# Kernel tuning notes

Hardware: AMD Instinct MI355X
Metric: run time of the kernel (lower is better)

The kernel has to match this reference:

```python
import jax, jax.numpy as jnp
import numpy as np

NUM_RAYS = 65536
N_COARSE = 64
INTERS_FINE = 128


def setup_inputs() -> dict:
    key = jax.random.key(0)
    k1, k2, k3 = jax.random.split(key, 3)
    weights = jax.random.uniform(k1, (NUM_RAYS, N_COARSE), dtype=jnp.float32)
    # sorted bin edges in [2, 6), turned into contiguous intervals [start, end]
    t_edges = jnp.sort(2.0 + 4.0 * jax.random.uniform(k2, (NUM_RAYS, N_COARSE + 1), dtype=jnp.float32), axis=-1)
    t_inters = jnp.stack([t_edges[:, :-1], t_edges[:, 1:]], axis=-1)  # [R, N, 2]
    # stratified jittered u, exactly as the original np.random construction
    eps32 = np.finfo(np.float32).eps
    s = 1.0 / (INTERS_FINE + 1)
    base = jnp.arange(INTERS_FINE + 1, dtype=jnp.float32) * s  # [F+1]
    jitter = jax.random.uniform(k3, (NUM_RAYS, INTERS_FINE + 1), dtype=jnp.float32,
                                minval=0.0, maxval=s - eps32)
    u = jnp.minimum(base[None, :] + jitter, 1.0 - eps32)
    return {"weights": weights, "t_inters": t_inters, "u": u}


def reference(weights, t_inters, u):
    eps = 1e-05
    num_rays = weights.shape[0]
    # maxblur of weights (mip-NeRF style) + floor
    wp = jnp.concatenate([weights[:, :1], weights, weights[:, -1:]], axis=-1)
    wmax = jnp.maximum(wp[:, :-1], wp[:, 1:])
    w = (wmax[:, :-1] + wmax[:, 1:]) * 0.5 + 0.01  # [R, N]
    # bin edges
    t_vals = jnp.concatenate([t_inters[..., 0], t_inters[:, -1:, 1]], axis=-1)  # [R, N+1]
    # normalize to pdf with eps padding
    wsum = jnp.sum(w, axis=-1, keepdims=True)
    padding = jnp.maximum(0.0, eps - wsum)
    w = w + padding / w.shape[-1]
    wsum = wsum + padding
    pdf = w / wsum
    cdf = jnp.minimum(1.0, jnp.cumsum(pdf[..., :-1], axis=-1))
    cdf = jnp.concatenate([jnp.zeros((num_rays, 1), jnp.float32), cdf,
                           jnp.ones((num_rays, 1), jnp.float32)], axis=-1)  # [R, N+1]
    # inverse CDF: the original's broadcast mask + max/min reductions are exactly
    # searchsorted(cdf, u, side='right'); idx-1 = last bin with cdf <= u (since
    # cdf[:,0]=0 <= u and u < 1 = cdf[:,-1], indices are always interior).
    idx = jax.vmap(lambda c, uu: jnp.searchsorted(c, uu, side='right'))(cdf, u)  # [R, F+1]
    last = cdf.shape[-1] - 1
    i0 = jnp.clip(idx - 1, 0, last)
    i1 = jnp.clip(idx, 0, last)
    cdf_g0 = jnp.take_along_axis(cdf, i0, axis=-1)
    cdf_g1 = jnp.take_along_axis(cdf, i1, axis=-1)
    bins_g0 = jnp.take_along_axis(t_vals, i0, axis=-1)
    bins_g1 = jnp.take_along_axis(t_vals, i1, axis=-1)
    t = (u - cdf_g0) / (cdf_g1 - cdf_g0)
    t = jnp.where(jnp.isnan(t), 0.0, t)  # matches t[t != t] = 0
    t = jnp.clip(t, 0.0, 1.0)
    samples = bins_g0 + t * (bins_g1 - bins_g0)  # [R, F+1]
    samples = jax.lax.stop_gradient(samples)     # matches .detach()
    samples = jnp.sort(samples, axis=-1)
    return jnp.stack([samples[:, :-1], samples[:, 1:]], axis=-1)  # [R, F, 2]
```

## Files before the change

### kernel.cpp

```cpp
#include <hip/hip_runtime.h>


#define RAYS_PER_BLOCK 4

template <int CTRL, int ROW_MASK>
__device__ __forceinline__ float dpp_add(float x) {
    int sh = __builtin_amdgcn_update_dpp(0, __float_as_int(x), CTRL, ROW_MASK, 0xf, false);
    return x + __int_as_float(sh);
}

__device__ __forceinline__ float readlane_f(float v, int lane) {
    return __int_as_float(__builtin_amdgcn_readlane(__float_as_int(v), lane));
}

__device__ __forceinline__ float bperm(int byteaddr, float v) {
    return __int_as_float(__builtin_amdgcn_ds_bpermute(byteaddr, __float_as_int(v)));
}

__device__ __forceinline__ float invert_fast(float uu, float cdfv, float tix, float dtv,
                                             float c8, float c16, float c24, float c32,
                                             float c40, float c48, float c56) {
    int lo = 0;
    float clo = 0.0f, chi = 1.0f;
    bool g1 = (c32 <= uu);
    if (g1) { lo = 32; clo = c32; } else { chi = c32; }
    float cA = g1 ? c48 : c16;
    bool g2 = (cA <= uu);
    if (g2) { lo += 16; clo = cA; } else { chi = cA; }
    float pL = g1 ? c40 : c8;
    float pH = g1 ? c56 : c24;
    float cB = g2 ? pH : pL;
    bool g3 = (cB <= uu);
    if (g3) { lo += 8; clo = cB; } else { chi = cB; }
    int loB = lo << 2;
    {
        float c = bperm(loB + 12, cdfv);
        if (c <= uu) { loB += 16; clo = c; } else { chi = c; }
    }
    {
        float c = bperm(loB + 4, cdfv);
        if (c <= uu) { loB += 8; clo = c; } else { chi = c; }
    }
    {
        float c = bperm(loB, cdfv);
        if (c <= uu) { loB += 4; clo = c; } else { chi = c; }
    }
    float b0 = bperm(loB, tix);
    float dt = bperm(loB, dtv);
    float t = (uu - clo) * __builtin_amdgcn_rcpf(chi - clo);
    t = (t != t) ? 0.0f : t;
    return b0 + t * dt;
}

__global__ __launch_bounds__(64 * RAYS_PER_BLOCK)
void sample_pdf_kernel(const float* __restrict__ weights,
                       const float* __restrict__ t_inters,
                       const float* __restrict__ u,
                       float* __restrict__ out,
                       int R) {
    const int lane = threadIdx.x & 63;
    const int wave = threadIdx.x >> 6;
    const int ray  = blockIdx.x * RAYS_PER_BLOCK + wave;
    if (ray >= R) return;

    float  w  = weights[(long)ray * 64 + lane];
    float2 ti = ((const float2*)t_inters)[(long)ray * 64 + lane];
    const float* ub = u + (long)ray * 129;
    float u0 = ub[lane];
    float u1 = ub[lane + 64];
    float u2 = ub[128];

    float wm1 = __shfl_up(w, 1, 64);
    float wp1 = __shfl_down(w, 1, 64);
    if (lane == 0)  wm1 = w;
    if (lane == 63) wp1 = w;
    float w2 = (fmaxf(wm1, w) + fmaxf(w, wp1)) * 0.5f + 0.01f;

    float scan = w2;
    scan = dpp_add<0x111, 0xf>(scan);
    scan = dpp_add<0x112, 0xf>(scan);
    scan = dpp_add<0x114, 0xf>(scan);
    scan = dpp_add<0x118, 0xf>(scan);
    scan = dpp_add<0x142, 0xa>(scan);
    scan = dpp_add<0x143, 0xc>(scan);

    float wsum    = readlane_f(scan, 63);
    float padding = fmaxf(0.0f, 1e-5f - wsum);
    float invden  = __builtin_amdgcn_rcpf(wsum + padding);
    float cdfv    = fminf(1.0f, (scan + (float)(lane + 1) * (padding * (1.0f / 64.0f))) * invden);
    if (lane == 63) cdfv = 1.0f;

    float nx  = __shfl_down(ti.x, 1, 64);
    float dtv = ((lane == 63) ? ti.y : nx) - ti.x;

    float c8  = readlane_f(cdfv, 7),  c16 = readlane_f(cdfv, 15);
    float c24 = readlane_f(cdfv, 23), c32 = readlane_f(cdfv, 31);
    float c40 = readlane_f(cdfv, 39), c48 = readlane_f(cdfv, 47);
    float c56 = readlane_f(cdfv, 55);

    float s0 = invert_fast(u0, cdfv, ti.x, dtv, c8, c16, c24, c32, c40, c48, c56);
    float s1 = invert_fast(u1, cdfv, ti.x, dtv, c8, c16, c24, c32, c40, c48, c56);

    unsigned long long mask = __ballot(cdfv <= u2);
    int l2 = __builtin_amdgcn_readfirstlane(__popcll(mask));
    float clo2 = (l2 == 0) ? 0.0f : readlane_f(cdfv, (l2 - 1) & 63);
    float chi2 = readlane_f(cdfv, l2);
    float b02  = readlane_f(ti.x, l2);
    float dt2  = readlane_f(dtv,  l2);
    float t2 = (u2 - clo2) * __builtin_amdgcn_rcpf(chi2 - clo2);
    t2 = (t2 != t2) ? 0.0f : t2;
    float s2 = b02 + t2 * dt2;

    float n0 = __shfl_down(s0, 1, 64);
    if (lane == 63) n0 = readlane_f(s1, 0);
    float n1 = __shfl_down(s1, 1, 64);
    if (lane == 63) n1 = s2;

    float2* o = ((float2*)out) + (long)ray * 128;
    o[lane]      = make_float2(s0, n0);
    o[lane + 64] = make_float2(s1, n1);
}

extern "C" void kernel_launch(void* const* d_in, const int* in_sizes, int n_in,
                              void* d_out, int out_size, void* d_ws, size_t ws_size,
                              hipStream_t stream) {
    const float* weights  = (const float*)d_in[0];
    const float* t_inters = (const float*)d_in[1];
    const float* u        = (const float*)d_in[2];
    float* out            = (float*)d_out;

    const int R = in_sizes[0] / 64;
    const int grid = (R + RAYS_PER_BLOCK - 1) / RAYS_PER_BLOCK;
    sample_pdf_kernel<<<grid, 64 * RAYS_PER_BLOCK, 0, stream>>>(weights, t_inters, u, out, R);
}
```

Baseline: 30.82 us.

## Precompute per-bin affine coefficients, interleave sample ownership, use wave DPP shifts

```diff
diff --git a/kernel.cpp b/kernel.cpp
--- a/kernel.cpp
+++ b/kernel.cpp
@@ -2,11 +2,19 @@
 
 
 #define RAYS_PER_BLOCK 4
+#define DPP_WAVE_SHL1 0x130
+#define DPP_WAVE_SHR1 0x138
 
 template <int CTRL, int ROW_MASK>
 __device__ __forceinline__ float dpp_add(float x) {
     int sh = __builtin_amdgcn_update_dpp(0, __float_as_int(x), CTRL, ROW_MASK, 0xf, false);
     return x + __int_as_float(sh);
+}
+
+template <int CTRL>
+__device__ __forceinline__ float dpp_old_f(float old, float src) {
+    return __int_as_float(__builtin_amdgcn_update_dpp(
+        __float_as_int(old), __float_as_int(src), CTRL, 0xf, 0xf, false));
 }
 
 __device__ __forceinline__ float readlane_f(float v, int lane) {
@@ -17,39 +25,25 @@
     return __int_as_float(__builtin_amdgcn_ds_bpermute(byteaddr, __float_as_int(v)));
 }
 
-__device__ __forceinline__ float invert_fast(float uu, float cdfv, float tix, float dtv,
-                                             float c8, float c16, float c24, float c32,
-                                             float c40, float c48, float c56) {
-    int lo = 0;
-    float clo = 0.0f, chi = 1.0f;
+__device__ __forceinline__ int search6(float uu, float cdfv,
+                                       float c8, float c16, float c24, float c32,
+                                       float c40, float c48, float c56) {
     bool g1 = (c32 <= uu);
-    if (g1) { lo = 32; clo = c32; } else { chi = c32; }
+    int loB = g1 ? 128 : 0;
     float cA = g1 ? c48 : c16;
     bool g2 = (cA <= uu);
-    if (g2) { lo += 16; clo = cA; } else { chi = cA; }
+    loB += g2 ? 64 : 0;
     float pL = g1 ? c40 : c8;
     float pH = g1 ? c56 : c24;
     float cB = g2 ? pH : pL;
-    bool g3 = (cB <= uu);
-    if (g3) { lo += 8; clo = cB; } else { chi = cB; }
-    int loB = lo << 2;
-    {
-        float c = bperm(loB + 12, cdfv);
-        if (c <= uu) { loB += 16; clo = c; } else { chi = c; }
-    }
-    {
-        float c = bperm(loB + 4, cdfv);
-        if (c <= uu) { loB += 8; clo = c; } else { chi = c; }
-    }
-    {
-        float c = bperm(loB, cdfv);
-        if (c <= uu) { loB += 4; clo = c; } else { chi = c; }
-    }
-    float b0 = bperm(loB, tix);
-    float dt = bperm(loB, dtv);
-    float t = (uu - clo) * __builtin_amdgcn_rcpf(chi - clo);
-    t = (t != t) ? 0.0f : t;
-    return b0 + t * dt;
+    loB += (cB <= uu) ? 32 : 0;
+    float c = bperm(loB + 12, cdfv);
+    loB += (c <= uu) ? 16 : 0;
+    c = bperm(loB + 4, cdfv);
+    loB += (c <= uu) ? 8 : 0;
+    c = bperm(loB, cdfv);
+    loB += (c <= uu) ? 4 : 0;
+    return loB;
 }
 
 __global__ __launch_bounds__(64 * RAYS_PER_BLOCK)
@@ -66,14 +60,12 @@
     float  w  = weights[(long)ray * 64 + lane];
     float2 ti = ((const float2*)t_inters)[(long)ray * 64 + lane];
     const float* ub = u + (long)ray * 129;
-    float u0 = ub[lane];
-    float u1 = ub[lane + 64];
+    float u0 = ub[2 * lane];
+    float u1 = ub[2 * lane + 1];
     float u2 = ub[128];
 
-    float wm1 = __shfl_up(w, 1, 64);
-    float wp1 = __shfl_down(w, 1, 64);
-    if (lane == 0)  wm1 = w;
-    if (lane == 63) wp1 = w;
+    float wm1 = dpp_old_f<DPP_WAVE_SHR1>(w, w);
+    float wp1 = dpp_old_f<DPP_WAVE_SHL1>(w, w);
     float w2 = (fmaxf(wm1, w) + fmaxf(w, wp1)) * 0.5f + 0.01f;
 
     float scan = w2;
@@ -84,41 +76,34 @@
     scan = dpp_add<0x142, 0xa>(scan);
     scan = dpp_add<0x143, 0xc>(scan);
 
-    float wsum    = readlane_f(scan, 63);
-    float padding = fmaxf(0.0f, 1e-5f - wsum);
-    float invden  = __builtin_amdgcn_rcpf(wsum + padding);
-    float cdfv    = fminf(1.0f, (scan + (float)(lane + 1) * (padding * (1.0f / 64.0f))) * invden);
+    float wsum = readlane_f(scan, 63);
+    float cdfv = fminf(1.0f, scan * __builtin_amdgcn_rcpf(wsum));
     if (lane == 63) cdfv = 1.0f;
 
-    float nx  = __shfl_down(ti.x, 1, 64);
-    float dtv = ((lane == 63) ? ti.y : nx) - ti.x;
+    float clo = dpp_old_f<DPP_WAVE_SHR1>(0.0f, cdfv);
+    float nx  = dpp_old_f<DPP_WAVE_SHL1>(ti.y, ti.x);
+    float dt  = nx - ti.x;
+    float Bv  = dt * __builtin_amdgcn_rcpf(cdfv - clo);
+    float Av  = ti.x - clo * Bv;
 
     float c8  = readlane_f(cdfv, 7),  c16 = readlane_f(cdfv, 15);
     float c24 = readlane_f(cdfv, 23), c32 = readlane_f(cdfv, 31);
     float c40 = readlane_f(cdfv, 39), c48 = readlane_f(cdfv, 47);
     float c56 = readlane_f(cdfv, 55);
 
-    float s0 = invert_fast(u0, cdfv, ti.x, dtv, c8, c16, c24, c32, c40, c48, c56);
-    float s1 = invert_fast(u1, cdfv, ti.x, dtv, c8, c16, c24, c32, c40, c48, c56);
+    int lA = search6(u0, cdfv, c8, c16, c24, c32, c40, c48, c56);
+    int lB = search6(u1, cdfv, c8, c16, c24, c32, c40, c48, c56);
+    float s_a = bperm(lA, Av) + bperm(lA, Bv) * u0;
+    float s_b = bperm(lB, Av) + bperm(lB, Bv) * u1;
 
     unsigned long long mask = __ballot(cdfv <= u2);
-    int l2 = __builtin_amdgcn_readfirstlane(__popcll(mask));
-    float clo2 = (l2 == 0) ? 0.0f : readlane_f(cdfv, (l2 - 1) & 63);
-    float chi2 = readlane_f(cdfv, l2);
-    float b02  = readlane_f(ti.x, l2);
-    float dt2  = readlane_f(dtv,  l2);
-    float t2 = (u2 - clo2) * __builtin_amdgcn_rcpf(chi2 - clo2);
-    t2 = (t2 != t2) ? 0.0f : t2;
-    float s2 = b02 + t2 * dt2;
+    int p = __popcll(mask);
+    float s2 = readlane_f(Av, p) + readlane_f(Bv, p) * u2;
 
-    float n0 = __shfl_down(s0, 1, 64);
-    if (lane == 63) n0 = readlane_f(s1, 0);
-    float n1 = __shfl_down(s1, 1, 64);
-    if (lane == 63) n1 = s2;
+    float s_an = dpp_old_f<DPP_WAVE_SHL1>(s2, s_a);
 
-    float2* o = ((float2*)out) + (long)ray * 128;
-    o[lane]      = make_float2(s0, n0);
-    o[lane + 64] = make_float2(s1, n1);
+    float4 o4 = make_float4(s_a, s_b, s_b, s_an);
+    ((float4*)out)[(long)ray * 64 + lane] = o4;
 }
 
 extern "C" void kernel_launch(void* const* d_in, const int* in_sizes, int n_in,
```

After: 28.08 us. 1.1x faster.
